# Optimization experiments

Measured on AMD Instinct MI355X. Metric: run time of the kernel, lower is better.

Reference implementation:

```python
import jax, jax.numpy as jnp
import numpy as np

N, D, H = 4096, 256, 8
DH = D // H
E = 131072
LN_EPS = 1e-5
NEG = -1e9


def setup_inputs() -> dict:
    key = jax.random.key(0)
    ks = jax.random.split(key, 10)
    s = 0.02
    return {
        "embeddings": jax.random.normal(ks[0], (N, D), dtype=jnp.float32),
        "edge_index": jax.random.randint(ks[1], (2, E), 0, N, dtype=jnp.int64),
        "in_proj_w": jax.random.normal(ks[2], (3 * D, D), dtype=jnp.float32) * s,
        "in_proj_b": jnp.zeros((3 * D,), jnp.float32),
        "out_w": jax.random.normal(ks[3], (D, D), dtype=jnp.float32) * s,
        "out_b": jnp.zeros((D,), jnp.float32),
        "lin_w": jax.random.normal(ks[4], (D, D), dtype=jnp.float32) * s,
        "lin_b": jnp.zeros((D,), jnp.float32),
        "ln_g": jnp.ones((D,), jnp.float32),
        "ln_beta": jnp.zeros((D,), jnp.float32),
    }


def reference(embeddings, edge_index, in_proj_w, in_proj_b, out_w, out_b, lin_w, lin_b, ln_g, ln_beta):
    n, d = embeddings.shape
    src, dst = edge_index[0], edge_index[1]
    # symmetric adjacency (per-cell neighbor set = unique nodes touching the cell),
    # self excluded (matches `neighbor_indices != cell_idx`)
    adj = jnp.zeros((n, n), dtype=bool).at[src, dst].set(True).at[dst, src].set(True)
    adj = adj & ~jnp.eye(n, dtype=bool)
    has_nb = adj.any(axis=1)  # [N]

    # MultiheadAttention (eval: dropout off), single query per cell over its neighbors
    qkv = embeddings @ in_proj_w.T + in_proj_b          # [N, 3D]
    q, k, v = jnp.split(qkv, 3, axis=-1)
    qh = q.reshape(n, H, DH)
    kh = k.reshape(n, H, DH)
    vh = v.reshape(n, H, DH)
    scale = 1.0 / np.sqrt(DH).astype(np.float32)
    scores = jnp.einsum('nhd,mhd->nhm', qh, kh) * scale  # [N, H, N]
    scores = jnp.where(adj[:, None, :], scores, NEG)
    attn = jax.nn.softmax(scores, axis=-1)
    ctx = jnp.einsum('nhm,mhd->nhd', attn, vh).reshape(n, d)
    ctx = ctx @ out_w.T + out_b
    # cells with no neighbors keep their own embedding
    x = jnp.where(has_nb[:, None], ctx, embeddings)

    # context_transform: Linear -> LayerNorm -> GELU (dropout off in eval)
    y = x @ lin_w.T + lin_b
    mu = y.mean(axis=-1, keepdims=True)
    var = y.var(axis=-1, keepdims=True)
    y = (y - mu) / jnp.sqrt(var + LN_EPS) * ln_g + ln_beta
    return jax.nn.gelu(y, approximate=False)
```

## Files before the change

kernel.cpp:

```cpp
#include <hip/hip_runtime.h>
#include <math.h>

#define NN 4096
#define DD 256
#define EE 131072
#define MAXD 128
#define SP 132

typedef __attribute__((ext_vector_type(8))) short short8;
typedef __attribute__((ext_vector_type(4))) float float4v;

__device__ __forceinline__ unsigned short f2bf(float f){
    unsigned u = __float_as_uint(f);
    return (unsigned short)((u + 0x7fffu + ((u >> 16) & 1u)) >> 16);
}
__device__ __forceinline__ float blo(unsigned u){ return __uint_as_float(u << 16); }
__device__ __forceinline__ float bhi(unsigned u){ return __uint_as_float(u & 0xffff0000u); }

__device__ __forceinline__ void pack_one(const float* __restrict__ src, unsigned short* __restrict__ dst, int e){
    int lane = e & 63;
    int row = ((e >> 9) << 4) + (lane & 15);
    int k0 = ((e >> 6) & 7) * 32 + ((lane >> 4) << 3);
    const float* p = src + row * DD + k0;
    short8 v;
    #pragma unroll
    for (int j = 0; j < 8; ++j) v[j] = (short)f2bf(p[j]);
    ((short8*)dst)[e] = v;
}

__global__ void k_packw(const float* __restrict__ ipw, const float* __restrict__ ow, const float* __restrict__ lw,
                        unsigned short* __restrict__ bipw, unsigned short* __restrict__ bow,
                        unsigned short* __restrict__ blw, unsigned* __restrict__ adj){
    int e = blockIdx.x * 256 + threadIdx.x;
    for (int i = e; i < 524288; i += 40960) adj[i] = 0u;
    if (e < 24576)       pack_one(ipw, bipw, e);
    else if (e < 32768)  pack_one(ow,  bow,  e - 24576);
    else                 pack_one(lw,  blw,  e - 32768);
}

__global__ void __launch_bounds__(256) k_gqkv(const float* __restrict__ emb, const unsigned short* __restrict__ Bp,
                                              const float* __restrict__ bias, float* __restrict__ qf,
                                              unsigned short* __restrict__ kb, unsigned short* __restrict__ vb,
                                              const int* __restrict__ ei, unsigned* __restrict__ adj){
    __shared__ float sA[16 * 260];
    int bx = blockIdx.x, by = blockIdx.y;
    int t = threadIdx.x, w = t >> 6, lane = t & 63;

    int gid = (by * gridDim.x + bx) * 256 + t;
    if (gid < EE){
        int s = ei[gid], d = ei[EE + gid];
        if (s != d){
            atomicOr(&adj[s * 128 + (d >> 5)], 1u << (d & 31));
            atomicOr(&adj[d * 128 + (s >> 5)], 1u << (s & 31));
        }
    }

    #pragma unroll
    for (int i = 0; i < 16; ++i)
        sA[i * 260 + t] = emb[(bx * 16 + i) * 256 + t];
    __syncthreads();

    int arow = lane & 15, ak0 = (lane >> 4) << 3;
    short8 af[8];
    #pragma unroll
    for (int s = 0; s < 8; ++s){
        const float* p = &sA[arow * 260 + s * 32 + ak0];
        #pragma unroll
        for (int j = 0; j < 8; ++j) af[s][j] = (short)f2bf(p[j]);
    }

    const short8* B8 = (const short8*)Bp;
    float4v acc[4];
    #pragma unroll
    for (int c = 0; c < 4; ++c) acc[c] = (float4v){0.f, 0.f, 0.f, 0.f};
    #pragma unroll
    for (int s = 0; s < 8; ++s){
        #pragma unroll
        for (int c = 0; c < 4; ++c){
            int to = by * 16 + w * 4 + c;
            acc[c] = __builtin_amdgcn_mfma_f32_16x16x32_bf16(af[s], B8[(to * 8 + s) * 64 + lane], acc[c], 0, 0, 0);
        }
    }
    int q = lane >> 4, col = lane & 15;
    #pragma unroll
    for (int c = 0; c < 4; ++c){
        int o = (w * 4 + c) * 16 + col;
        float bo = bias[by * 256 + o];
        #pragma unroll
        for (int r = 0; r < 4; ++r){
            int node = bx * 16 + q * 4 + r;
            float val = acc[c][r] + bo;
            if (by == 0)      qf[node * 256 + o] = val;
            else if (by == 1) kb[node * 256 + o] = f2bf(val);
            else              vb[node * 256 + o] = f2bf(val);
        }
    }
}

__device__ __forceinline__ float dot32(const float4* qa, uint4 a, uint4 b, uint4 c, uint4 d){
    float s;
    s  = qa[0].x*blo(a.x) + qa[0].y*bhi(a.x) + qa[0].z*blo(a.y) + qa[0].w*bhi(a.y);
    s += qa[1].x*blo(a.z) + qa[1].y*bhi(a.z) + qa[1].z*blo(a.w) + qa[1].w*bhi(a.w);
    s += qa[2].x*blo(b.x) + qa[2].y*bhi(b.x) + qa[2].z*blo(b.y) + qa[2].w*bhi(b.y);
    s += qa[3].x*blo(b.z) + qa[3].y*bhi(b.z) + qa[3].z*blo(b.w) + qa[3].w*bhi(b.w);
    s += qa[4].x*blo(c.x) + qa[4].y*bhi(c.x) + qa[4].z*blo(c.y) + qa[4].w*bhi(c.y);
    s += qa[5].x*blo(c.z) + qa[5].y*bhi(c.z) + qa[5].z*blo(c.w) + qa[5].w*bhi(c.w);
    s += qa[6].x*blo(d.x) + qa[6].y*bhi(d.x) + qa[6].z*blo(d.y) + qa[6].w*bhi(d.y);
    s += qa[7].x*blo(d.z) + qa[7].y*bhi(d.z) + qa[7].z*blo(d.w) + qa[7].w*bhi(d.w);
    return s;
}

__global__ void __launch_bounds__(512) k_attn_tail(
        const float* __restrict__ qf, const unsigned short* __restrict__ kb,
        const unsigned short* __restrict__ vb, const unsigned* __restrict__ adj,
        const float* __restrict__ emb,
        const unsigned short* __restrict__ Bow, const float* __restrict__ ob,
        const unsigned short* __restrict__ Blw, const float* __restrict__ lb,
        const float* __restrict__ g, const float* __restrict__ beta,
        float* __restrict__ out){
    __shared__ float  sS[8][8][SP];
    __shared__ int    sNbr[8][MAXD];
    __shared__ short8 sPk[512];
    __shared__ float  sInv[8][8];
    __shared__ int    sDeg[16];
    __shared__ float  stat[16][2];
    int bx = blockIdx.x, t = threadIdx.x;
    int wv = t >> 6, lane = t & 63;
    int n0 = bx * 16;
    float* xs = (float*)sS;

    for (int u = 0; u < 2; ++u){
        int m = wv * 2 + u;
        int n = n0 + m;

        uint2 aw = ((const uint2*)(adj + n * 128))[lane];
        int cnt = __popc(aw.x) + __popc(aw.y);
        int pre = cnt;
        #pragma unroll
        for (int off = 1; off < 64; off <<= 1){
            int tmp = __shfl_up(pre, off);
            if (lane >= off) pre += tmp;
        }
        int tot = __shfl(pre, 63);
        int dg = (tot < MAXD) ? tot : MAXD;
        if (lane == 63) sDeg[m] = dg;
        int base = pre - cnt;
        int mb = lane * 64;
        unsigned b0 = aw.x, b1 = aw.y;
        while (b0){ int b = __ffs(b0) - 1; b0 &= b0 - 1u; if (base < MAXD) sNbr[wv][base] = mb + b; base++; }
        mb += 32;
        while (b1){ int b = __ffs(b1) - 1; b1 &= b1 - 1u; if (base < MAXD) sNbr[wv][base] = mb + b; base++; }
        if (dg == 0) continue;
        asm volatile("s_waitcnt lgkmcnt(0)" ::: "memory");

        int js = lane >> 3, h = lane & 7;
        float4 qa[8];
        const float4* q4 = (const float4*)(qf + n * 256 + h * 32);
        #pragma unroll
        for (int i = 0; i < 8; ++i) qa[i] = q4[i];
        for (int jb = 0; jb < dg; jb += 16){
            int j0 = jb + js, j1 = jb + 8 + js;
            bool v0 = j0 < dg, v1 = j1 < dg;
            int m0 = v0 ? sNbr[wv][j0] : sNbr[wv][0];
            int m1 = v1 ? sNbr[wv][j1] : sNbr[wv][0];
            const uint4* kr0 = (const uint4*)(kb + m0 * 256) + h * 4;
            const uint4* kr1 = (const uint4*)(kb + m1 * 256) + h * 4;
            uint4 a0 = kr0[0], a1 = kr0[1], a2 = kr0[2], a3 = kr0[3];
            uint4 c0 = kr1[0], c1 = kr1[1], c2 = kr1[2], c3 = kr1[3];
            float s0 = dot32(qa, a0, a1, a2, a3) * 0.17677669529663687f;
            float s1 = dot32(qa, c0, c1, c2, c3) * 0.17677669529663687f;
            if (v0) sS[wv][h][j0] = s0;
            if (v1) sS[wv][h][j1] = s1;
        }
        asm volatile("s_waitcnt lgkmcnt(0)" ::: "memory");

        int h2 = lane >> 3, i2 = lane & 7;
        float m1 = -1e30f;
        for (int j = i2; j < dg; j += 8) m1 = fmaxf(m1, sS[wv][h2][j]);
        m1 = fmaxf(m1, __shfl_xor(m1, 1));
        m1 = fmaxf(m1, __shfl_xor(m1, 2));
        m1 = fmaxf(m1, __shfl_xor(m1, 4));
        float sum = 0.f;
        for (int j = i2; j < dg; j += 8){ float e = __expf(sS[wv][h2][j] - m1); sS[wv][h2][j] = e; sum += e; }
        sum += __shfl_xor(sum, 1);
        sum += __shfl_xor(sum, 2);
        sum += __shfl_xor(sum, 4);
        if (i2 == 0) sInv[wv][h2] = 1.0f / sum;
        asm volatile("s_waitcnt lgkmcnt(0)" ::: "memory");

        int h3 = lane >> 3;
        const uint2* vb2 = (const uint2*)vb;
        float4 O = {0.f, 0.f, 0.f, 0.f};
        int j = 0;
        for (; j + 8 <= dg; j += 8){
            uint2 uu[8]; float ww[8];
            #pragma unroll
            for (int k = 0; k < 8; ++k){
                uu[k] = vb2[sNbr[wv][j + k] * 64 + lane];
                ww[k] = sS[wv][h3][j + k];
            }
            #pragma unroll
            for (int k = 0; k < 8; ++k){
                O.x += ww[k] * blo(uu[k].x); O.y += ww[k] * bhi(uu[k].x);
                O.z += ww[k] * blo(uu[k].y); O.w += ww[k] * bhi(uu[k].y);
            }
        }
        for (; j < dg; ++j){
            uint2 u = vb2[sNbr[wv][j] * 64 + lane];
            float wgt = sS[wv][h3][j];
            O.x += wgt * blo(u.x); O.y += wgt * bhi(u.x);
            O.z += wgt * blo(u.y); O.w += wgt * bhi(u.y);
        }
        float inv = sInv[wv][h3];

        int d0 = lane * 4;
        int s  = d0 >> 5;
        int l2 = ((d0 >> 3) & 3) * 16 + m;
        uint2 pk;
        pk.x = (unsigned)f2bf(O.x * inv) | ((unsigned)f2bf(O.y * inv) << 16);
        pk.y = (unsigned)f2bf(O.z * inv) | ((unsigned)f2bf(O.w * inv) << 16);
        ((uint2*)sPk)[(s * 64 + l2) * 2 + ((d0 & 7) >> 2)] = pk;
    }
    __syncthreads();

    const short8* B8 = (const short8*)Bow;
    float4v acc[2];
    #pragma unroll
    for (int c = 0; c < 2; ++c) acc[c] = (float4v){0.f, 0.f, 0.f, 0.f};
    #pragma unroll
    for (int s = 0; s < 8; ++s){
        short8 a = sPk[s * 64 + lane];
        #pragma unroll
        for (int c = 0; c < 2; ++c)
            acc[c] = __builtin_amdgcn_mfma_f32_16x16x32_bf16(a, B8[((wv * 2 + c) * 8 + s) * 64 + lane], acc[c], 0, 0, 0);
    }
    int q = lane >> 4, col = lane & 15;
    #pragma unroll
    for (int c = 0; c < 2; ++c){
        int o = (wv * 2 + c) * 16 + col;
        float bo = ob[o];
        #pragma unroll
        for (int r = 0; r < 4; ++r){
            int row = q * 4 + r;
            float x = acc[c][r] + bo;
            if (sDeg[row] == 0) x = emb[(n0 + row) * 256 + o];
            xs[row * 264 + o] = x;
        }
    }
    __syncthreads();

    {
        int l2 = t & 63, s = t >> 6;
        int m = l2 & 15, k0 = s * 32 + ((l2 >> 4) << 3);
        short8 v;
        #pragma unroll
        for (int j = 0; j < 8; ++j) v[j] = (short)f2bf(xs[m * 264 + k0 + j]);
        __syncthreads();
        sPk[t] = v;
    }
    __syncthreads();

    const short8* B2 = (const short8*)Blw;
    float4v acc2[2];
    #pragma unroll
    for (int c = 0; c < 2; ++c) acc2[c] = (float4v){0.f, 0.f, 0.f, 0.f};
    #pragma unroll
    for (int s = 0; s < 8; ++s){
        short8 a = sPk[s * 64 + lane];
        #pragma unroll
        for (int c = 0; c < 2; ++c)
            acc2[c] = __builtin_amdgcn_mfma_f32_16x16x32_bf16(a, B2[((wv * 2 + c) * 8 + s) * 64 + lane], acc2[c], 0, 0, 0);
    }
    __syncthreads();
    #pragma unroll
    for (int c = 0; c < 2; ++c){
        int o = (wv * 2 + c) * 16 + col;
        float bo = lb[o];
        #pragma unroll
        for (int r = 0; r < 4; ++r)
            xs[(q * 4 + r) * 264 + o] = acc2[c][r] + bo;
    }
    __syncthreads();

    int rr = t >> 5, i = t & 31;
    float s1 = 0.f, s2 = 0.f;
    #pragma unroll
    for (int jj = 0; jj < 8; ++jj){ float v = xs[rr * 264 + i + 32 * jj]; s1 += v; s2 += v * v; }
    #pragma unroll
    for (int off = 16; off > 0; off >>= 1){ s1 += __shfl_xor(s1, off); s2 += __shfl_xor(s2, off); }
    if (i == 0){
        float mu = s1 * (1.0f / 256.0f);
        float var = s2 * (1.0f / 256.0f) - mu * mu;
        stat[rr][0] = mu;
        stat[rr][1] = rsqrtf(fmaxf(var, 0.f) + 1e-5f);
    }
    __syncthreads();
    float mu = stat[rr][0], rs = stat[rr][1];
    int nbase = (n0 + rr) * 256;
    #pragma unroll
    for (int jj = 0; jj < 8; ++jj){
        int cc = i + 32 * jj;
        float z = (xs[rr * 264 + cc] - mu) * rs * g[cc] + beta[cc];
        out[nbase + cc] = 0.5f * z * (1.0f + erff(z * 0.70710678118654752f));
    }
}

extern "C" void kernel_launch(void* const* d_in, const int* in_sizes, int n_in,
                              void* d_out, int out_size, void* d_ws, size_t ws_size,
                              hipStream_t stream){
    const float* emb = (const float*)d_in[0];
    const int*   ei  = (const int*)d_in[1];
    const float* ipw = (const float*)d_in[2];
    const float* ipb = (const float*)d_in[3];
    const float* ow  = (const float*)d_in[4];
    const float* ob  = (const float*)d_in[5];
    const float* lw  = (const float*)d_in[6];
    const float* lb  = (const float*)d_in[7];
    const float* g   = (const float*)d_in[8];
    const float* bet = (const float*)d_in[9];

    char* ws = (char*)d_ws;
    unsigned*       adj  = (unsigned*)(ws);
    unsigned short* bipw = (unsigned short*)(ws + 2113536);
    unsigned short* bow  = (unsigned short*)(ws + 2506752);
    unsigned short* blw  = (unsigned short*)(ws + 2637824);
    float*          qf   = (float*)(ws + 2768896);
    unsigned short* kb   = (unsigned short*)(ws + 6963200);
    unsigned short* vb   = (unsigned short*)(ws + 9060352);

    k_packw    <<<160, 256, 0, stream>>>(ipw, ow, lw, bipw, bow, blw, adj);
    k_gqkv     <<<dim3(256, 3), 256, 0, stream>>>(emb, bipw, ipb, qf, kb, vb, ei, adj);
    k_attn_tail<<<256, 512, 0, stream>>>(qf, kb, vb, adj, emb, bow, ob, blw, lb, g, bet, (float*)d_out);
}
```

Measured before the change: 129.7 us.

## Process eight nodes per block to double grid size for attention tail

Each block now handles 8 nodes, one per wave, instead of 16 nodes with two sequential iterations per wave. The grid doubles to 512 blocks, spreading the gather-heavy attention phase across more CUs and removing the serial per-wave loop. The cost is that the 16-row MFMA projections now run half-empty with zero padding, and the weight loads for the two projections are repeated across twice as many blocks. LayerNorm is reworked to one row per wave using wave-level reductions, which removes a shared-memory stats pass and a barrier.

```diff
diff --git a/kernel.cpp b/kernel.cpp
--- a/kernel.cpp
+++ b/kernel.cpp
@@ -122,35 +122,32 @@
     __shared__ int    sNbr[8][MAXD];
     __shared__ short8 sPk[512];
     __shared__ float  sInv[8][8];
-    __shared__ int    sDeg[16];
-    __shared__ float  stat[16][2];
+    __shared__ int    sDeg[8];
     int bx = blockIdx.x, t = threadIdx.x;
     int wv = t >> 6, lane = t & 63;
-    int n0 = bx * 16;
+    int n0 = bx * 8;
+    int n = n0 + wv;
     float* xs = (float*)sS;
 
-    for (int u = 0; u < 2; ++u){
-        int m = wv * 2 + u;
-        int n = n0 + m;
-
-        uint2 aw = ((const uint2*)(adj + n * 128))[lane];
-        int cnt = __popc(aw.x) + __popc(aw.y);
-        int pre = cnt;
-        #pragma unroll
-        for (int off = 1; off < 64; off <<= 1){
-            int tmp = __shfl_up(pre, off);
-            if (lane >= off) pre += tmp;
-        }
-        int tot = __shfl(pre, 63);
-        int dg = (tot < MAXD) ? tot : MAXD;
-        if (lane == 63) sDeg[m] = dg;
-        int base = pre - cnt;
-        int mb = lane * 64;
-        unsigned b0 = aw.x, b1 = aw.y;
-        while (b0){ int b = __ffs(b0) - 1; b0 &= b0 - 1u; if (base < MAXD) sNbr[wv][base] = mb + b; base++; }
-        mb += 32;
-        while (b1){ int b = __ffs(b1) - 1; b1 &= b1 - 1u; if (base < MAXD) sNbr[wv][base] = mb + b; base++; }
-        if (dg == 0) continue;
+    uint2 aw = ((const uint2*)(adj + n * 128))[lane];
+    int cnt = __popc(aw.x) + __popc(aw.y);
+    int pre = cnt;
+    #pragma unroll
+    for (int off = 1; off < 64; off <<= 1){
+        int tmp = __shfl_up(pre, off);
+        if (lane >= off) pre += tmp;
+    }
+    int tot = __shfl(pre, 63);
+    int dg = (tot < MAXD) ? tot : MAXD;
+    if (lane == 63) sDeg[wv] = dg;
+    int base = pre - cnt;
+    int mb = lane * 64;
+    unsigned b0 = aw.x, b1 = aw.y;
+    while (b0){ int b = __ffs(b0) - 1; b0 &= b0 - 1u; if (base < MAXD) sNbr[wv][base] = mb + b; base++; }
+    mb += 32;
+    while (b1){ int b = __ffs(b1) - 1; b1 &= b1 - 1u; if (base < MAXD) sNbr[wv][base] = mb + b; base++; }
+
+    if (dg > 0){
         asm volatile("s_waitcnt lgkmcnt(0)" ::: "memory");
 
         int js = lane >> 3, h = lane & 7;
@@ -215,7 +212,7 @@
 
         int d0 = lane * 4;
         int s  = d0 >> 5;
-        int l2 = ((d0 >> 3) & 3) * 16 + m;
+        int l2 = ((d0 >> 3) & 3) * 16 + wv;
         uint2 pk;
         pk.x = (unsigned)f2bf(O.x * inv) | ((unsigned)f2bf(O.y * inv) << 16);
         pk.y = (unsigned)f2bf(O.z * inv) | ((unsigned)f2bf(O.w * inv) << 16);
@@ -242,20 +239,26 @@
         #pragma unroll
         for (int r = 0; r < 4; ++r){
             int row = q * 4 + r;
-            float x = acc[c][r] + bo;
-            if (sDeg[row] == 0) x = emb[(n0 + row) * 256 + o];
-            xs[row * 264 + o] = x;
+            if (row < 8){
+                float x = acc[c][r] + bo;
+                if (sDeg[row] == 0) x = emb[(n0 + row) * 256 + o];
+                xs[row * 264 + o] = x;
+            }
         }
     }
     __syncthreads();
 
     {
         int l2 = t & 63, s = t >> 6;
-        int m = l2 & 15, k0 = s * 32 + ((l2 >> 4) << 3);
+        int mm = l2 & 15, k0 = s * 32 + ((l2 >> 4) << 3);
         short8 v;
-        #pragma unroll
-        for (int j = 0; j < 8; ++j) v[j] = (short)f2bf(xs[m * 264 + k0 + j]);
-        __syncthreads();
+        if (mm < 8){
+            #pragma unroll
+            for (int j = 0; j < 8; ++j) v[j] = (short)f2bf(xs[mm * 264 + k0 + j]);
+        } else {
+            #pragma unroll
+            for (int j = 0; j < 8; ++j) v[j] = 0;
+        }
         sPk[t] = v;
     }
     __syncthreads();
@@ -277,30 +280,27 @@
         int o = (wv * 2 + c) * 16 + col;
         float bo = lb[o];
         #pragma unroll
-        for (int r = 0; r < 4; ++r)
-            xs[(q * 4 + r) * 264 + o] = acc2[c][r] + bo;
-    }
-    __syncthreads();
-
-    int rr = t >> 5, i = t & 31;
+        for (int r = 0; r < 4; ++r){
+            int row = q * 4 + r;
+            if (row < 8) xs[row * 264 + o] = acc2[c][r] + bo;
+        }
+    }
+    __syncthreads();
+
+    int i = lane;
     float s1 = 0.f, s2 = 0.f;
     #pragma unroll
-    for (int jj = 0; jj < 8; ++jj){ float v = xs[rr * 264 + i + 32 * jj]; s1 += v; s2 += v * v; }
-    #pragma unroll
-    for (int off = 16; off > 0; off >>= 1){ s1 += __shfl_xor(s1, off); s2 += __shfl_xor(s2, off); }
-    if (i == 0){
-        float mu = s1 * (1.0f / 256.0f);
-        float var = s2 * (1.0f / 256.0f) - mu * mu;
-        stat[rr][0] = mu;
-        stat[rr][1] = rsqrtf(fmaxf(var, 0.f) + 1e-5f);
-    }
-    __syncthreads();
-    float mu = stat[rr][0], rs = stat[rr][1];
-    int nbase = (n0 + rr) * 256;
-    #pragma unroll
-    for (int jj = 0; jj < 8; ++jj){
-        int cc = i + 32 * jj;
-        float z = (xs[rr * 264 + cc] - mu) * rs * g[cc] + beta[cc];
+    for (int jj = 0; jj < 4; ++jj){ float v = xs[wv * 264 + i + 64 * jj]; s1 += v; s2 += v * v; }
+    #pragma unroll
+    for (int off = 32; off > 0; off >>= 1){ s1 += __shfl_xor(s1, off); s2 += __shfl_xor(s2, off); }
+    float mu = s1 * (1.0f / 256.0f);
+    float var = s2 * (1.0f / 256.0f) - mu * mu;
+    float rs = rsqrtf(fmaxf(var, 0.f) + 1e-5f);
+    int nbase = (n0 + wv) * 256;
+    #pragma unroll
+    for (int jj = 0; jj < 4; ++jj){
+        int cc = i + 64 * jj;
+        float z = (xs[wv * 264 + cc] - mu) * rs * g[cc] + beta[cc];
         out[nbase + cc] = 0.5f * z * (1.0f + erff(z * 0.70710678118654752f));
     }
 }
@@ -330,5 +330,5 @@
 
     k_packw    <<<160, 256, 0, stream>>>(ipw, ow, lw, bipw, bow, blw, adj);
     k_gqkv     <<<dim3(256, 3), 256, 0, stream>>>(emb, bipw, ipb, qf, kb, vb, ei, adj);
-    k_attn_tail<<<256, 512, 0, stream>>>(qf, kb, vb, adj, emb, bow, ob, blw, lb, g, bet, (float*)d_out);
-}
+    k_attn_tail<<<512, 512, 0, stream>>>(qf, kb, vb, adj, emb, bow, ob, blw, lb, g, bet, (float*)d_out);
+}
```

Result: faster. 125.1 us (-3.6%).
